# Optimization experiments

Hardware: AMD Instinct MI355X
Metric: run time of the kernel (lower is better)

The kernel has to match this reference:

```python
import jax, jax.numpy as jnp
import numpy as np

N = 8192
D = 512

def _row_normalize(m):
    # row-normalize; rows summing to 0 get inverse 0 (inf -> 0 in original)
    rs = m.sum(axis=1, keepdims=True)
    inv = jnp.where(rs == 0, 0.0, 1.0 / rs)
    return m * inv

def setup_inputs() -> dict:
    key = jax.random.key(0)
    k1, k2 = jax.random.split(key)
    qf = jax.random.normal(k1, (N, D), dtype=jnp.float32)
    gf = jax.random.normal(k2, (N, D), dtype=jnp.float32)
    return {"qf": qf, "gf": gf}

def reference(qf, gf):
    # feature = row-normalized squared difference  [N, D]
    feature = _row_normalize((qf - gf) ** 2)
    # adj[i, j] = ||feature_i - feature_j||^2, via GEMM expansion
    sq = jnp.sum(feature * feature, axis=-1)                  # [N]
    adj = sq[:, None] + sq[None, :] - 2.0 * (feature @ feature.T)  # [N, N]
    # symmetrize: elementwise max(adj, adj.T) (equivalent to the masked mix)
    adj = jnp.maximum(adj, adj.T)
    # add identity and row-normalize
    adj = adj + jnp.eye(N, dtype=adj.dtype)
    adj = _row_normalize(adj)
    return adj, feature
```

## Files before the change

### kernel.cpp

```cpp
#include <hip/hip_runtime.h>
#include <hip/hip_bf16.h>

#define N 8192
#define D 512

typedef __attribute__((ext_vector_type(8))) short short8;
typedef __attribute__((ext_vector_type(4))) float f32x4;

__device__ __forceinline__ float block_reduce_256(float v, float* red) {
    #pragma unroll
    for (int o = 1; o < 64; o <<= 1) v += __shfl_xor(v, o, 64);
    int w = threadIdx.x >> 6;
    if ((threadIdx.x & 63) == 0) red[w] = v;
    __syncthreads();
    float tot = red[0] + red[1] + red[2] + red[3];
    __syncthreads();
    return tot;
}

__global__ void feature_kernel(const float* __restrict__ qf, const float* __restrict__ gf,
                               float* __restrict__ feat, __hip_bfloat16* __restrict__ featb,
                               float* __restrict__ sq) {
    __shared__ float red[4];
    int row = blockIdx.x, t = threadIdx.x;
    const float2* q2 = (const float2*)(qf + (size_t)row * D);
    const float2* g2 = (const float2*)(gf + (size_t)row * D);
    float2 qv = q2[t], gv = g2[t];
    float a = qv.x - gv.x, b = qv.y - gv.y;
    float va = a * a, vb = b * b;
    float rs = block_reduce_256(va + vb, red);
    float inv = (rs == 0.0f) ? 0.0f : 1.0f / rs;
    float fa = va * inv, fb = vb * inv;
    ((float2*)(feat + (size_t)row * D))[t] = make_float2(fa, fb);
    __hip_bfloat162 h;
    h.x = __float2bfloat16(fa);
    h.y = __float2bfloat16(fb);
    ((__hip_bfloat162*)(featb + (size_t)row * D))[t] = h;
    float tot = block_reduce_256(fa * fa + fb * fb, red);
    if (t == 0) sq[row] = tot;
}

__global__ void colsum_partial_kernel(const float* __restrict__ feat, float* __restrict__ partial) {
    int b = blockIdx.x, t = threadIdx.x;
    const float* fp = feat + (size_t)b * 128 * D;
    float a0 = 0.f, a1 = 0.f;
    for (int r = 0; r < 128; ++r) {
        a0 += fp[r * D + t];
        a1 += fp[r * D + t + 256];
    }
    partial[b * D + t] = a0;
    partial[b * D + t + 256] = a1;
}

__global__ void finalize_kernel(const float* __restrict__ partial, const float* __restrict__ sq,
                                float* __restrict__ cvec, float* __restrict__ Sval) {
    __shared__ float red[4];
    int t = threadIdx.x;
    if (blockIdx.x == 0) {
        float a0 = 0.f, a1 = 0.f;
        for (int b = 0; b < 64; ++b) {
            a0 += partial[b * D + t];
            a1 += partial[b * D + t + 256];
        }
        cvec[t] = a0;
        cvec[t + 256] = a1;
    } else {
        float s = 0.f;
        for (int k = 0; k < N / 256; ++k) s += sq[t + 256 * k];
        float tot = block_reduce_256(s, red);
        if (t == 0) Sval[0] = tot;
    }
}

__global__ void rowinv_kernel(const float* __restrict__ feat, const float* __restrict__ sq,
                              const float* __restrict__ cvec, const float* __restrict__ Sval,
                              float* __restrict__ rowinv) {
    __shared__ float red[4];
    int row = blockIdx.x, t = threadIdx.x;
    float2 f = ((const float2*)(feat + (size_t)row * D))[t];
    float2 c = ((const float2*)cvec)[t];
    float dot = block_reduce_256(f.x * c.x + f.y * c.y, red);
    if (t == 0) {
        float rs = (float)N * sq[row] + Sval[0] - 2.0f * dot + 1.0f;
        rowinv[row] = (rs == 0.0f) ? 0.0f : 1.0f / rs;
    }
}

__global__ __launch_bounds__(256, 2) void adj_gemm_kernel(const __hip_bfloat16* __restrict__ featb,
                                                          const float* __restrict__ sq,
                                                          const float* __restrict__ rowinv,
                                                          float* __restrict__ out) {
    __shared__ __align__(16) char lds[16384];
    int wg = blockIdx.x;
    int swz = (wg & 7) * 512 + (wg >> 3);
    int bx = swz & 63, by = swz >> 6;
    int rowBase = by * 128, colBase = bx * 128;
    int t = threadIdx.x, lane = t & 63, w = t >> 6;
    int wr = w >> 1, wc = w & 1;

    f32x4 acc[4][4];
    #pragma unroll
    for (int m = 0; m < 4; ++m)
        #pragma unroll
        for (int n = 0; n < 4; ++n) acc[m][n] = (f32x4){0.f, 0.f, 0.f, 0.f};

    int r0 = t >> 2, cc = t & 3;
    int s0 = (r0 >> 1) & 3;
    int woff = r0 * 64 + ((cc ^ s0) * 16);
    const __hip_bfloat16* gA0 = featb + (size_t)(rowBase + r0) * D + cc * 8;
    const __hip_bfloat16* gB0 = featb + (size_t)(colBase + r0) * D + cc * 8;
    char* ldsA = lds;
    char* ldsB = lds + 8192;

    for (int ks = 0; ks < D / 32; ++ks) {
        int k0 = ks * 32;
        short8 vA0 = *(const short8*)(gA0 + k0);
        short8 vA1 = *(const short8*)(gA0 + 64 * D + k0);
        short8 vB0 = *(const short8*)(gB0 + k0);
        short8 vB1 = *(const short8*)(gB0 + 64 * D + k0);
        *(short8*)(ldsA + woff)        = vA0;
        *(short8*)(ldsA + woff + 4096) = vA1;
        *(short8*)(ldsB + woff)        = vB0;
        *(short8*)(ldsB + woff + 4096) = vB1;
        __syncthreads();

        short8 afrag[4], bfrag[4];
        #pragma unroll
        for (int m = 0; m < 4; ++m) {
            int r = wr * 64 + m * 16 + (lane & 15);
            int c16 = (lane >> 4) ^ ((r >> 1) & 3);
            afrag[m] = *(const short8*)(ldsA + r * 64 + c16 * 16);
        }
        #pragma unroll
        for (int n = 0; n < 4; ++n) {
            int r = wc * 64 + n * 16 + (lane & 15);
            int c16 = (lane >> 4) ^ ((r >> 1) & 3);
            bfrag[n] = *(const short8*)(ldsB + r * 64 + c16 * 16);
        }
        #pragma unroll
        for (int m = 0; m < 4; ++m)
            #pragma unroll
            for (int n = 0; n < 4; ++n)
                acc[m][n] = __builtin_amdgcn_mfma_f32_16x16x32_bf16(afrag[m], bfrag[n], acc[m][n], 0, 0, 0);
        __syncthreads();
    }

    float sqj[4];
    int jcol[4];
    #pragma unroll
    for (int n = 0; n < 4; ++n) {
        jcol[n] = colBase + wc * 64 + n * 16 + (lane & 15);
        sqj[n] = sq[jcol[n]];
    }
    #pragma unroll
    for (int m = 0; m < 4; ++m) {
        int ibase = rowBase + wr * 64 + m * 16 + ((lane >> 4) << 2);
        #pragma unroll
        for (int r = 0; r < 4; ++r) {
            int i = ibase + r;
            float si = sq[i], ri = rowinv[i];
            size_t rowoff = (size_t)i * N;
            #pragma unroll
            for (int n = 0; n < 4; ++n) {
                float pre = si + sqj[n] - 2.0f * acc[m][n][r] + (i == jcol[n] ? 1.0f : 0.0f);
                out[rowoff + jcol[n]] = pre * ri;
            }
        }
    }
}

extern "C" void kernel_launch(void* const* d_in, const int* in_sizes, int n_in,
                              void* d_out, int out_size, void* d_ws, size_t ws_size,
                              hipStream_t stream) {
    const float* qf = (const float*)d_in[0];
    const float* gf = (const float*)d_in[1];
    float* out = (float*)d_out;
    float* feat = out + (size_t)N * N;

    char* wsb = (char*)d_ws;
    __hip_bfloat16* featb = (__hip_bfloat16*)wsb;
    float* sq      = (float*)(wsb + 8388608);
    float* partial = (float*)(wsb + 8388608 + 32768);
    float* cvec    = (float*)(wsb + 8388608 + 32768 + 131072);
    float* Sval    = (float*)(wsb + 8388608 + 32768 + 131072 + 2048);
    float* rowinv  = (float*)(wsb + 8388608 + 32768 + 131072 + 2048 + 64);

    feature_kernel<<<N, 256, 0, stream>>>(qf, gf, feat, featb, sq);
    colsum_partial_kernel<<<64, 256, 0, stream>>>(feat, partial);
    finalize_kernel<<<2, 256, 0, stream>>>(partial, sq, cvec, Sval);
    rowinv_kernel<<<N, 256, 0, stream>>>(feat, sq, cvec, Sval, rowinv);
    adj_gemm_kernel<<<4096, 256, 0, stream>>>(featb, sq, rowinv, out);
}
```

Before: 151.8 us.

## Compute only upper-triangular GEMM tiles and mirror them via LDS transpose

Exploits symmetry of the pairwise distance matrix so that only the 2080 upper-triangular 128x128 tiles are computed. Each off-diagonal tile writes its own block, then transposes the pre-normalization values through LDS and writes the mirrored block scaled by the other row's inverse sum. This roughly halves the MFMA and global-read work. The K loop also moves to 64-wide steps with register-staged double-buffered LDS prefetch. The cost is 72KB of LDS per block, which may limit occupancy, plus an extra epilogue pass. The dominant 256MB output write is unchanged.

Result: faster. 124.8 us (-17.8%).

```diff
diff --git a/kernel.cpp b/kernel.cpp
--- a/kernel.cpp
+++ b/kernel.cpp
@@ -86,17 +86,23 @@
     }
 }
 
-__global__ __launch_bounds__(256, 2) void adj_gemm_kernel(const __hip_bfloat16* __restrict__ featb,
-                                                          const float* __restrict__ sq,
-                                                          const float* __restrict__ rowinv,
-                                                          float* __restrict__ out) {
-    __shared__ __align__(16) char lds[16384];
+__global__ __launch_bounds__(256, 2) void adj_gemm_sym_kernel(const __hip_bfloat16* __restrict__ featb,
+                                                              const float* __restrict__ sq,
+                                                              const float* __restrict__ rowinv,
+                                                              float* __restrict__ out) {
+    __shared__ __align__(16) char lds[73728];
     int wg = blockIdx.x;
-    int swz = (wg & 7) * 512 + (wg >> 3);
-    int bx = swz & 63, by = swz >> 6;
+    int id = (wg & 7) * 260 + (wg >> 3);
+    int r = (int)((129.0f - sqrtf(16641.0f - 8.0f * (float)id)) * 0.5f);
+    if (r > 63) r = 63;
+    while (r > 0 && (r * (129 - r)) / 2 > id) --r;
+    while (((r + 1) * (128 - r)) / 2 <= id) ++r;
+    int by = r;
+    int bx = r + (id - (r * (129 - r)) / 2);
     int rowBase = by * 128, colBase = bx * 128;
+
     int t = threadIdx.x, lane = t & 63, w = t >> 6;
-    int wr = w >> 1, wc = w & 1;
+    int wr = w >> 1, wc = w & 1, g = lane >> 4;
 
     f32x4 acc[4][4];
     #pragma unroll
@@ -104,47 +110,70 @@
         #pragma unroll
         for (int n = 0; n < 4; ++n) acc[m][n] = (f32x4){0.f, 0.f, 0.f, 0.f};
 
-    int r0 = t >> 2, cc = t & 3;
-    int s0 = (r0 >> 1) & 3;
-    int woff = r0 * 64 + ((cc ^ s0) * 16);
-    const __hip_bfloat16* gA0 = featb + (size_t)(rowBase + r0) * D + cc * 8;
-    const __hip_bfloat16* gB0 = featb + (size_t)(colBase + r0) * D + cc * 8;
-    char* ldsA = lds;
-    char* ldsB = lds + 8192;
-
-    for (int ks = 0; ks < D / 32; ++ks) {
-        int k0 = ks * 32;
-        short8 vA0 = *(const short8*)(gA0 + k0);
-        short8 vA1 = *(const short8*)(gA0 + 64 * D + k0);
-        short8 vB0 = *(const short8*)(gB0 + k0);
-        short8 vB1 = *(const short8*)(gB0 + 64 * D + k0);
-        *(short8*)(ldsA + woff)        = vA0;
-        *(short8*)(ldsA + woff + 4096) = vA1;
-        *(short8*)(ldsB + woff)        = vB0;
-        *(short8*)(ldsB + woff + 4096) = vB1;
+    int srow = t >> 3, schunk = t & 7;
+    const __hip_bfloat16* gA = featb + (size_t)(rowBase + srow) * D + schunk * 8;
+    const __hip_bfloat16* gB = featb + (size_t)(colBase + srow) * D + schunk * 8;
+    int wo0 = srow * 128 + ((schunk ^ (srow & 7)) * 16);
+
+    int arow = wr * 64 + (lane & 15);
+    int brow = wc * 64 + (lane & 15);
+    int swzc = lane & 7;
+    int ca0 = ((g) ^ swzc) * 16, ca1 = ((4 + g) ^ swzc) * 16;
+
+    short8 ra[4], rb[4];
+    #pragma unroll
+    for (int q = 0; q < 4; ++q) {
+        ra[q] = *(const short8*)(gA + (size_t)q * 32 * D);
+        rb[q] = *(const short8*)(gB + (size_t)q * 32 * D);
+    }
+    #pragma unroll
+    for (int q = 0; q < 4; ++q) {
+        *(short8*)(lds + wo0 + q * 4096) = ra[q];
+        *(short8*)(lds + 32768 + wo0 + q * 4096) = rb[q];
+    }
+    __syncthreads();
+
+    int cur = 0;
+    for (int ks = 0; ks < 8; ++ks) {
+        if (ks < 7) {
+            int k0 = (ks + 1) * 64;
+            #pragma unroll
+            for (int q = 0; q < 4; ++q) {
+                ra[q] = *(const short8*)(gA + (size_t)q * 32 * D + k0);
+                rb[q] = *(const short8*)(gB + (size_t)q * 32 * D + k0);
+            }
+        }
+        short8 af[4][2], bf[4][2];
+        const char* pA = lds + (cur << 14);
+        const char* pB = lds + 32768 + (cur << 14);
+        #pragma unroll
+        for (int m = 0; m < 4; ++m) {
+            af[m][0] = *(const short8*)(pA + (arow + 16 * m) * 128 + ca0);
+            af[m][1] = *(const short8*)(pA + (arow + 16 * m) * 128 + ca1);
+            bf[m][0] = *(const short8*)(pB + (brow + 16 * m) * 128 + ca0);
+            bf[m][1] = *(const short8*)(pB + (brow + 16 * m) * 128 + ca1);
+        }
+        #pragma unroll
+        for (int m = 0; m < 4; ++m)
+            #pragma unroll
+            for (int n = 0; n < 4; ++n) {
+                acc[m][n] = __builtin_amdgcn_mfma_f32_16x16x32_bf16(af[m][0], bf[n][0], acc[m][n], 0, 0, 0);
+                acc[m][n] = __builtin_amdgcn_mfma_f32_16x16x32_bf16(af[m][1], bf[n][1], acc[m][n], 0, 0, 0);
+            }
+        if (ks < 7) {
+            char* wA = lds + ((cur ^ 1) << 14);
+            char* wB = lds + 32768 + ((cur ^ 1) << 14);
+            #pragma unroll
+            for (int q = 0; q < 4; ++q) {
+                *(short8*)(wA + wo0 + q * 4096) = ra[q];
+                *(short8*)(wB + wo0 + q * 4096) = rb[q];
+            }
+        }
         __syncthreads();
-
-        short8 afrag[4], bfrag[4];
-        #pragma unroll
-        for (int m = 0; m < 4; ++m) {
-            int r = wr * 64 + m * 16 + (lane & 15);
-            int c16 = (lane >> 4) ^ ((r >> 1) & 3);
-            afrag[m] = *(const short8*)(ldsA + r * 64 + c16 * 16);
-        }
-        #pragma unroll
-        for (int n = 0; n < 4; ++n) {
-            int r = wc * 64 + n * 16 + (lane & 15);
-            int c16 = (lane >> 4) ^ ((r >> 1) & 3);
-            bfrag[n] = *(const short8*)(ldsB + r * 64 + c16 * 16);
-        }
-        #pragma unroll
-        for (int m = 0; m < 4; ++m)
-            #pragma unroll
-            for (int n = 0; n < 4; ++n)
-                acc[m][n] = __builtin_amdgcn_mfma_f32_16x16x32_bf16(afrag[m], bfrag[n], acc[m][n], 0, 0, 0);
-        __syncthreads();
-    }
-
+        cur ^= 1;
+    }
+
+    float* T = (float*)(lds + w * 18432);
     float sqj[4];
     int jcol[4];
     #pragma unroll
@@ -152,19 +181,38 @@
         jcol[n] = colBase + wc * 64 + n * 16 + (lane & 15);
         sqj[n] = sq[jcol[n]];
     }
+    int offdiag = (by != bx);
     #pragma unroll
     for (int m = 0; m < 4; ++m) {
-        int ibase = rowBase + wr * 64 + m * 16 + ((lane >> 4) << 2);
-        #pragma unroll
-        for (int r = 0; r < 4; ++r) {
-            int i = ibase + r;
+        int ibase = rowBase + wr * 64 + m * 16 + g * 4;
+        #pragma unroll
+        for (int rI = 0; rI < 4; ++rI) {
+            int i = ibase + rI;
             float si = sq[i], ri = rowinv[i];
-            size_t rowoff = (size_t)i * N;
+            size_t ro = (size_t)i * N;
             #pragma unroll
             for (int n = 0; n < 4; ++n) {
-                float pre = si + sqj[n] - 2.0f * acc[m][n][r] + (i == jcol[n] ? 1.0f : 0.0f);
-                out[rowoff + jcol[n]] = pre * ri;
-            }
+                float pre = si + sqj[n] - 2.0f * acc[m][n][rI] + (i == jcol[n] ? 1.0f : 0.0f);
+                out[ro + jcol[n]] = pre * ri;
+                if (offdiag) {
+                    int ii = m * 16 + g * 4 + rI;
+                    int jj = n * 16 + (lane & 15);
+                    T[jj * 72 + ii] = pre;
+                }
+            }
+        }
+    }
+    if (offdiag) {
+        __syncthreads();
+        #pragma unroll
+        for (int it = 0; it < 16; ++it) {
+            int jj = it * 4 + g;
+            int ii0 = (lane & 15) * 4;
+            f32x4 v = *(const f32x4*)&T[jj * 72 + ii0];
+            int j = colBase + wc * 64 + jj;
+            float rj = rowinv[j];
+            v *= rj;
+            *(f32x4*)&out[(size_t)j * N + rowBase + wr * 64 + ii0] = v;
         }
     }
 }
@@ -189,5 +237,5 @@
     colsum_partial_kernel<<<64, 256, 0, stream>>>(feat, partial);
     finalize_kernel<<<2, 256, 0, stream>>>(partial, sq, cvec, Sval);
     rowinv_kernel<<<N, 256, 0, stream>>>(feat, sq, cvec, Sval, rowinv);
-    adj_gemm_kernel<<<4096, 256, 0, stream>>>(featb, sq, rowinv, out);
-}
+    adj_gemm_sym_kernel<<<2080, 256, 0, stream>>>(featb, sq, rowinv, out);
+}
```

## Compute only upper-triangular GEMM tiles and mirror results into transposed tiles

Applied to the files above, without the earlier changes.

Exploits symmetry of the distance matrix: launches 2080 upper-triangle tiles instead of 4096, decoding tile coordinates via a sqrt-based triangular index, and each off-diagonal tile also writes its transposed block scaled by the column row-inverse. This is meant to roughly halve the MFMA work and fragment loads. In exchange, the transposed writes are 16-byte column-oriented stores that scatter across many rows, so the output write pattern is less coalesced. Occupancy hint is also raised from 2 to 3 blocks per CU.

After: 124.9 us. 17.7% less time.

```diff
diff --git a/kernel.cpp b/kernel.cpp
--- a/kernel.cpp
+++ b/kernel.cpp
@@ -86,17 +86,23 @@
     }
 }
 
-__global__ __launch_bounds__(256, 2) void adj_gemm_kernel(const __hip_bfloat16* __restrict__ featb,
-                                                          const float* __restrict__ sq,
-                                                          const float* __restrict__ rowinv,
-                                                          float* __restrict__ out) {
+__global__ __launch_bounds__(256, 3) void adj_gemm_sym_kernel(const __hip_bfloat16* __restrict__ featb,
+                                                              const float* __restrict__ sq,
+                                                              const float* __restrict__ rowinv,
+                                                              float* __restrict__ out) {
     __shared__ __align__(16) char lds[16384];
     int wg = blockIdx.x;
-    int swz = (wg & 7) * 512 + (wg >> 3);
-    int bx = swz & 63, by = swz >> 6;
+    int id = (wg & 7) * 260 + (wg >> 3);
+    int r = (int)((129.0f - sqrtf(16641.0f - 8.0f * (float)id)) * 0.5f);
+    if (r > 63) r = 63;
+    while (r > 0 && (r * (129 - r)) / 2 > id) --r;
+    while (((r + 1) * (128 - r)) / 2 <= id) ++r;
+    int by = r;
+    int bx = r + (id - (r * (129 - r)) / 2);
     int rowBase = by * 128, colBase = bx * 128;
+
     int t = threadIdx.x, lane = t & 63, w = t >> 6;
-    int wr = w >> 1, wc = w & 1;
+    int wr = w >> 1, wc = w & 1, g = lane >> 4;
 
     f32x4 acc[4][4];
     #pragma unroll
@@ -127,15 +133,15 @@
         short8 afrag[4], bfrag[4];
         #pragma unroll
         for (int m = 0; m < 4; ++m) {
-            int r = wr * 64 + m * 16 + (lane & 15);
-            int c16 = (lane >> 4) ^ ((r >> 1) & 3);
-            afrag[m] = *(const short8*)(ldsA + r * 64 + c16 * 16);
+            int rr = wr * 64 + m * 16 + (lane & 15);
+            int c16 = (lane >> 4) ^ ((rr >> 1) & 3);
+            afrag[m] = *(const short8*)(ldsA + rr * 64 + c16 * 16);
         }
         #pragma unroll
         for (int n = 0; n < 4; ++n) {
-            int r = wc * 64 + n * 16 + (lane & 15);
-            int c16 = (lane >> 4) ^ ((r >> 1) & 3);
-            bfrag[n] = *(const short8*)(ldsB + r * 64 + c16 * 16);
+            int rr = wc * 64 + n * 16 + (lane & 15);
+            int c16 = (lane >> 4) ^ ((rr >> 1) & 3);
+            bfrag[n] = *(const short8*)(ldsB + rr * 64 + c16 * 16);
         }
         #pragma unroll
         for (int m = 0; m < 4; ++m)
@@ -145,25 +151,38 @@
         __syncthreads();
     }
 
-    float sqj[4];
+    float sqj[4], rj4[4];
     int jcol[4];
     #pragma unroll
     for (int n = 0; n < 4; ++n) {
         jcol[n] = colBase + wc * 64 + n * 16 + (lane & 15);
         sqj[n] = sq[jcol[n]];
-    }
+        rj4[n] = rowinv[jcol[n]];
+    }
+    int offdiag = (by != bx);
     #pragma unroll
     for (int m = 0; m < 4; ++m) {
-        int ibase = rowBase + wr * 64 + m * 16 + ((lane >> 4) << 2);
-        #pragma unroll
-        for (int r = 0; r < 4; ++r) {
-            int i = ibase + r;
-            float si = sq[i], ri = rowinv[i];
-            size_t rowoff = (size_t)i * N;
-            #pragma unroll
-            for (int n = 0; n < 4; ++n) {
-                float pre = si + sqj[n] - 2.0f * acc[m][n][r] + (i == jcol[n] ? 1.0f : 0.0f);
-                out[rowoff + jcol[n]] = pre * ri;
+        int i0 = rowBase + wr * 64 + m * 16 + g * 4;
+        float si0 = sq[i0], si1 = sq[i0 + 1], si2 = sq[i0 + 2], si3 = sq[i0 + 3];
+        float ri0 = rowinv[i0], ri1 = rowinv[i0 + 1], ri2 = rowinv[i0 + 2], ri3 = rowinv[i0 + 3];
+        #pragma unroll
+        for (int n = 0; n < 4; ++n) {
+            int j = jcol[n];
+            float pre0 = si0 + sqj[n] - 2.0f * acc[m][n][0] + (i0 == j ? 1.0f : 0.0f);
+            float pre1 = si1 + sqj[n] - 2.0f * acc[m][n][1] + (i0 + 1 == j ? 1.0f : 0.0f);
+            float pre2 = si2 + sqj[n] - 2.0f * acc[m][n][2] + (i0 + 2 == j ? 1.0f : 0.0f);
+            float pre3 = si3 + sqj[n] - 2.0f * acc[m][n][3] + (i0 + 3 == j ? 1.0f : 0.0f);
+            out[(size_t)(i0 + 0) * N + j] = pre0 * ri0;
+            out[(size_t)(i0 + 1) * N + j] = pre1 * ri1;
+            out[(size_t)(i0 + 2) * N + j] = pre2 * ri2;
+            out[(size_t)(i0 + 3) * N + j] = pre3 * ri3;
+            if (offdiag) {
+                f32x4 v;
+                v[0] = pre0 * rj4[n];
+                v[1] = pre1 * rj4[n];
+                v[2] = pre2 * rj4[n];
+                v[3] = pre3 * rj4[n];
+                *(f32x4*)&out[(size_t)j * N + i0] = v;
             }
         }
     }
@@ -189,5 +208,5 @@
     colsum_partial_kernel<<<64, 256, 0, stream>>>(feat, partial);
     finalize_kernel<<<2, 256, 0, stream>>>(partial, sq, cvec, Sval);
     rowinv_kernel<<<N, 256, 0, stream>>>(feat, sq, cvec, Sval, rowinv);
-    adj_gemm_kernel<<<4096, 256, 0, stream>>>(featb, sq, rowinv, out);
-}
+    adj_gemm_sym_kernel<<<2080, 256, 0, stream>>>(featb, sq, rowinv, out);
+}
```
